# Performance work log

Hardware: AMD Instinct MI355X
Metric: run time of the kernel (lower is better)

Reference implementation:

```python
import jax, jax.numpy as jnp
import numpy as np

B, S, H, E, V = 32, 256, 512, 300, 32000
ALEN, LLEN, POL = 4, 16, 3
HOP, LAM = 10, 0.01


def _layernorm(x, g, b, eps=1e-12):
    mu = jnp.mean(x, -1, keepdims=True)
    var = jnp.mean((x - mu) ** 2, -1, keepdims=True)
    return (x - mu) / jnp.sqrt(var + eps) * g + b


def _pos_weight(x, a0, a1, text_len, aspect_len):
    # vectorized version of ASGCN_NEW.position_weight
    j = jnp.arange(x.shape[1])[None, :]
    cl = (text_len - aspect_len).astype(jnp.float32)[:, None]
    a0b, a1b, tlb = a0[:, None], a1[:, None], text_len[:, None]
    w = jnp.where(j < a0b, 1.0 - (a0b - j) / cl,
        jnp.where(j <= a1b, 0.0,
        jnp.where(j < tlb, 1.0 - (j - a1b) / cl, 0.0)))
    return w[:, :, None] * x


def _mask(x, a0, a1):
    j = jnp.arange(x.shape[1])[None, :]
    m = ((j >= a0[:, None]) & (j <= a1[:, None])).astype(x.dtype)
    return m[:, :, None] * x


def _gcn(x, adj, w, b):
    h = jnp.einsum('bsh,hk->bsk', x, w)
    denom = jnp.sum(adj, 2, keepdims=True) + 1.0
    return jnp.einsum('bst,bth->bsh', adj, h) / denom + b


def _conv1d(x, w, b):
    # x: [B,S,C] -> conv over S with kernel 3, pad 1 -> [B,S,C]
    y = jax.lax.conv_general_dilated(jnp.swapaxes(x, 1, 2), w, (1,), ((1, 1),),
                                     dimension_numbers=('NCH', 'OIH', 'NCH'))
    return jnp.swapaxes(y + b[None, :, None], 1, 2)


def _lstm_dir(x, mask, wih, whh, b, reverse):
    # masked LSTM matching pack_padded semantics: state frozen / output zero at pad
    xs = jnp.swapaxes(x, 0, 1)       # [S,B,E]
    ms = jnp.swapaxes(mask, 0, 1)    # [S,B] bool
    if reverse:
        xs, ms = xs[::-1], ms[::-1]
    pre = jnp.einsum('sbe,ge->sbg', xs, wih) + b
    h0 = jnp.zeros((x.shape[0], whh.shape[1]), x.dtype)

    def step(carry, inp):
        h, c = carry
        p, m = inp
        g = p + h @ whh.T
        i, f, gg, o = jnp.split(g, 4, -1)
        c_new = jax.nn.sigmoid(f) * c + jax.nn.sigmoid(i) * jnp.tanh(gg)
        h_new = jax.nn.sigmoid(o) * jnp.tanh(c_new)
        m_ = m[:, None]
        return (jnp.where(m_, h_new, h), jnp.where(m_, c_new, c)), jnp.where(m_, h_new, 0.0)

    _, ys = jax.lax.scan(step, (h0, h0), (pre, ms))
    if reverse:
        ys = ys[::-1]
    return jnp.swapaxes(ys, 0, 1)


def _hop_attend(m, text_out, g, b):
    tT = jnp.swapaxes(text_out, 1, 2)
    for _ in range(HOP - 1):
        alpha = jnp.einsum('bsh,bht->bst', m, tT)          # [B,S,S]
        a = jnp.einsum('bst,bth->bsh', alpha, text_out)    # [B,S,H]
        m = LAM * _layernorm(jax.nn.sigmoid(a), g, b) + m
    alpha_mat = jnp.einsum('bsh,bht->bst', m, tT)
    alpha = jax.nn.softmax(jnp.sum(alpha_mat, 1, keepdims=True), axis=2)  # [B,1,S]
    return jnp.einsum('bot,bth->boh', alpha, text_out)[:, 0]              # [B,H]


def setup_inputs() -> dict:
    key = jax.random.key(0)
    ks = jax.random.split(key, 20)
    sc = 0.05
    text_indices = jax.random.randint(ks[0], (B, S), 1, V)
    aspect_indices = jax.random.randint(ks[1], (B, ALEN), 1, V)
    left_indices = jax.random.randint(ks[2], (B, LLEN), 1, V)
    adj = (jax.random.uniform(ks[3], (B, S, S)) < 0.1).astype(jnp.float32)
    adj = jnp.minimum(adj + jnp.eye(S, dtype=jnp.float32)[None], 1.0)
    return {
        'text_indices': text_indices,
        'aspect_indices': aspect_indices,
        'left_indices': left_indices,
        'adj': adj,
        'embedding': jax.random.normal(ks[4], (V, E)) * sc,
        'lstm_wih_f': jax.random.normal(ks[5], (4 * H, E)) * sc,
        'lstm_whh_f': jax.random.normal(ks[6], (4 * H, H)) * sc,
        'lstm_b_f': jnp.zeros((4 * H,), jnp.float32),
        'lstm_wih_b': jax.random.normal(ks[7], (4 * H, E)) * sc,
        'lstm_whh_b': jax.random.normal(ks[8], (4 * H, H)) * sc,
        'lstm_b_b': jnp.zeros((4 * H,), jnp.float32),
        'gc_w': jax.random.normal(ks[9], (6, H, H)) * sc,
        'gc_b': jnp.zeros((6, H), jnp.float32),
        'conv1_w': jax.random.normal(ks[10], (H, H, 3)) * sc,
        'conv1_b': jnp.zeros((H,), jnp.float32),
        'conv2_w': jax.random.normal(ks[11], (H, H, 3)) * sc,
        'conv2_b': jnp.zeros((H,), jnp.float32),
        'fc2_w': jax.random.normal(ks[12], (POL, 3 * H)) * sc,
        'fc2_b': jnp.zeros((POL,), jnp.float32),
        'ln_g': jnp.ones((3, H), jnp.float32),
        'ln_b': jnp.zeros((3, H), jnp.float32),
    }


def _forward(text_indices, aspect_indices, left_indices, adj, embedding,
             lstm_wih_f, lstm_whh_f, lstm_b_f, lstm_wih_b, lstm_whh_b, lstm_b_b,
             gc_w, gc_b, conv1_w, conv1_b, conv2_w, conv2_b, fc2_w, fc2_b, ln_g, ln_b):
    text_len = jnp.sum(text_indices != 0, -1)
    aspect_len = jnp.sum(aspect_indices != 0, -1)
    left_len = jnp.sum(left_indices != 0, -1)
    a0 = left_len
    a1 = left_len + aspect_len - 1
    text = embedding[text_indices]  # dropout identity in eval mode
    m = text_indices != 0
    hf = _lstm_dir(text, m, lstm_wih_f, lstm_whh_f, lstm_b_f, False)
    hb = _lstm_dir(text, m, lstm_wih_b, lstm_whh_b, lstm_b_b, True)
    # concat fwd/bwd then reshape(B,S,H,2).mean(-1), exactly as the torch code
    text_out = jnp.concatenate([hf, hb], -1).reshape(B, S, H, 2).mean(-1)

    pw = lambda t: _pos_weight(t, a0, a1, text_len, aspect_len)

    x_conv = jax.nn.relu(_conv1d(pw(text_out), conv1_w, conv1_b))
    x_conv = jax.nn.relu(_conv1d(pw(x_conv), conv2_w, conv2_b))

    x = jax.nn.relu(_gcn(pw(text_out), adj, gc_w[0], gc_b[0]))
    pwx = pw(x)
    graph_mask = jnp.zeros_like(x)
    for k in range(1, 6):
        graph_mask = graph_mask + _mask(jax.nn.relu(_gcn(pwx, adj, gc_w[k], gc_b[k])), a0, a1)

    a1_vec = _hop_attend(graph_mask, text_out, ln_g[0], ln_b[0])
    a2_vec = _hop_attend(_mask(text_out, a0, a1), text_out, ln_g[1], ln_b[1])
    a3_vec = _hop_attend(_mask(x_conv, a0, a1), text_out, ln_g[2], ln_b[2])

    fnout = jnp.concatenate([a1_vec, a2_vec, a3_vec], 1)  # [B, 3H]
    return fnout @ fc2_w.T + fc2_b


def reference(text_indices, aspect_indices, left_indices, adj, embedding,
              lstm_wih_f, lstm_whh_f, lstm_b_f, lstm_wih_b, lstm_whh_b, lstm_b_b,
              gc_w, gc_b, conv1_w, conv1_b, conv2_w, conv2_b, fc2_w, fc2_b, ln_g, ln_b):
    return _forward(text_indices, aspect_indices, left_indices, adj, embedding,
                    lstm_wih_f, lstm_whh_f, lstm_b_f, lstm_wih_b, lstm_whh_b, lstm_b_b,
                    gc_w, gc_b, conv1_w, conv1_b, conv2_w, conv2_b, fc2_w, fc2_b, ln_g, ln_b)
```

## Files before the change

kernel.cpp:

```cpp
#include <hip/hip_runtime.h>
#include <hip/hip_fp16.h>

typedef unsigned int u32;
typedef unsigned long long u64;

static constexpr size_t OFF_X2    = 0;
static constexpr size_t OFF_PRE   = 9830400;
static constexpr size_t OFF_MB    = 131072;
static constexpr size_t OFF_FLG   = 135168;
static constexpr size_t OFF_TOUT  = 0;
static constexpr size_t OFF_TOUTT = 16777216;
static constexpr size_t OFF_PWT   = 33554432;
static constexpr size_t OFF_PWTTH = 50331648;
static constexpr size_t OFF_PWTTL = 58720256;
static constexpr size_t OFF_Y     = 76939264;
static constexpr size_t OFF_AGG0  = 76939264;
static constexpr size_t OFF_GCWT  = 93716480;
static constexpr size_t OFF_PWX   = 110493696;
static constexpr size_t OFF_WD    = 127270912;
static constexpr size_t OFF_WIH   = 131465216;
static constexpr size_t OFF_BIA   = 136380416;
static constexpr size_t OFF_W1T   = 136396800;
static constexpr size_t OFF_W2T   = 139542528;
static constexpr size_t OFF_META  = 142688256;
// ... 163 lines not shown

    const int srow = tid >> 4;
    const int sj   = tid & 15;

    for (int kb = 0; kb < 10; ++kb) {
        #pragma unroll
        for (int i = 0; i < 8; ++i) {
            int row = srow + i*16;
            As2[sj*132 + row] = X2u[(size_t)(m0 + row)*160 + kb*16 + sj];
            Bs2[sj*132 + row] = Wihu[(size_t)(n0 + row)*160 + kb*16 + sj];
        }
        __syncthreads();

        U4H8 bf[4];
        #pragma unroll
        for (int nt = 0; nt < 4; ++nt) {
            int col = wn*64 + nt*16 + l15;
            bf[nt].u = make_uint4(Bs2[(2*q)*132 + col], Bs2[(2*q+1)*132 + col],
                                  Bs2[(2*q+8)*132 + col], Bs2[(2*q+9)*132 + col]);
        }
        #pragma unroll
        for (int mt = 0; mt < 4; ++mt) {
            int row = wm*64 + mt*16 + l15;
            U4H8 af;
            af.u = make_uint4(As2[(2*q)*132 + row], As2[(2*q+1)*132 + row],
                              As2[(2*q+8)*132 + row], As2[(2*q+9)*132 + row]);
            #pragma unroll
            for (int nt = 0; nt < 4; ++nt)
                acc[mt][nt] = __builtin_amdgcn_mfma_f32_16x16x32_f16(af.h, bf[nt].h, acc[mt][nt], 0, 0, 0);
        }
        __syncthreads();
    }

    #pragma unroll
    for (int nt = 0; nt < 4; ++nt) {
        int col = n0 + wn*64 + nt*16 + l15;
        float bv = bias[col];
        #pragma unroll
        for (int mt = 0; mt < 4; ++mt) {
            int rbase = m0 + wm*64 + mt*16 + q*4;
            #pragma unroll
            for (int p = 0; p < 4; ++p)
                pre[(size_t)(rbase + p)*4096 + col] = __float2half(acc[mt][nt][p] + bv);
        }
    }
}

template<int SPLITA, int EPI>
__global__ __launch_bounds__(256)
void mmsplit_k(const float* __restrict__ A, const u32* __restrict__ Bhi,
               const u32* __restrict__ Blo, float* __restrict__ C,
               int N, int Ku32, long sA, long sB, long sC,
               const float* __restrict__ bias, const float* __restrict__ denom,
               const float* __restrict__ posw)
{
    __shared__ u32 Ah[16*132];
    __shared__ u32 Al[16*132];
    __shared__ u32 Bh[16*132];
    __shared__ u32 Bl[16*132];
    const int z = blockIdx.z;
    A   += (size_t)z * sA;
    Bhi += (size_t)z * sB;
    Blo += (size_t)z * sB;
    C   += (size_t)z * sC;
    const int m0 = blockIdx.x * 128;
    const int n0 = blockIdx.y * 128;
    const int tid = threadIdx.x;
    const int wv = tid >> 6;
    const int l  = tid & 63;
    const int q  = l >> 4;
    const int l15 = l & 15;
    const int wm = wv & 1, wn = wv >> 1;
    const int pitchA = 2*Ku32;

    f32x4 acc[4][4];
    #pragma unroll
    for (int mt = 0; mt < 4; ++mt)
        #pragma unroll
        for (int nt = 0; nt < 4; ++nt)
            acc[mt][nt] = (f32x4){0.f, 0.f, 0.f, 0.f};

    const int srow = tid >> 4;
    const int sj   = tid & 15;
    const int nkb = Ku32 >> 4;

    for (int kb = 0; kb < nkb; ++kb) {
        #pragma unroll
        for (int i = 0; i < 8; ++i) {
            int row = srow + i*16;
            float2 av = *(const float2*)(A + (size_t)(m0 + row)*pitchA + kb*32 + 2*sj);
            __half h0 = __float2half(av.x), h1 = __float2half(av.y);
            Ah[sj*132 + row] = (u32)__half_as_ushort(h0) | ((u32)__half_as_ushort(h1) << 16);
            if (SPLITA)
                Al[sj*132 + row] = packh2(av.x - __half2float(h0), av.y - __half2float(h1));
            Bh[sj*132 + row] = Bhi[(size_t)(n0 + row)*Ku32 + kb*16 + sj];
            Bl[sj*132 + row] = Blo[(size_t)(n0 + row)*Ku32 + kb*16 + sj];
        }
        __syncthreads();

        U4H8 bfh[4], bfl[4];
        #pragma unroll
        for (int nt = 0; nt < 4; ++nt) {
            int col = wn*64 + nt*16 + l15;
            bfh[nt].u = make_uint4(Bh[(2*q)*132 + col], Bh[(2*q+1)*132 + col],
                                   Bh[(2*q+8)*132 + col], Bh[(2*q+9)*132 + col]);
            bfl[nt].u = make_uint4(Bl[(2*q)*132 + col], Bl[(2*q+1)*132 + col],
                                   Bl[(2*q+8)*132 + col], Bl[(2*q+9)*132 + col]);
        }
        #pragma unroll
        for (int mt = 0; mt < 4; ++mt) {
            int row = wm*64 + mt*16 + l15;
            U4H8 afh;
            afh.u = make_uint4(Ah[(2*q)*132 + row], Ah[(2*q+1)*132 + row],
                               Ah[(2*q+8)*132 + row], Ah[(2*q+9)*132 + row]);
            #pragma unroll
            for (int nt = 0; nt < 4; ++nt) {
                acc[mt][nt] = __builtin_amdgcn_mfma_f32_16x16x32_f16(afh.h, bfh[nt].h, acc[mt][nt], 0, 0, 0);
                acc[mt][nt] = __builtin_amdgcn_mfma_f32_16x16x32_f16(afh.h, bfl[nt].h, acc[mt][nt], 0, 0, 0);
            }
            if (SPLITA) {
                U4H8 afl;
                afl.u = make_uint4(Al[(2*q)*132 + row], Al[(2*q+1)*132 + row],
                                   Al[(2*q+8)*132 + row], Al[(2*q+9)*132 + row]);
                #pragma unroll
                for (int nt = 0; nt < 4; ++nt)
                    acc[mt][nt] = __builtin_amdgcn_mfma_f32_16x16x32_f16(afl.h, bfh[nt].h, acc[mt][nt], 0, 0, 0);
            }
        }
        __syncthreads();
    }

    #pragma unroll
    for (int nt = 0; nt < 4; ++nt) {
        int col = n0 + wn*64 + nt*16 + l15;
        float bv = (EPI == 1) ? bias[col] : 0.f;
        #pragma unroll
        for (int mt = 0; mt < 4; ++mt) {
            int rbase = m0 + wm*64 + mt*16 + q*4;
            #pragma unroll
            for (int p = 0; p < 4; ++p) {
                int m = rbase + p;
                if (EPI == 0) {
                    C[(size_t)m*N + col] = acc[mt][nt][p];
                } else {
                    float v = fmaf(acc[mt][nt][p], 1.f/denom[m], bv);
                    C[(size_t)m*N + col] = fmaxf(v, 0.f) * posw[m];
                }
            }
        }
    }
}

__global__ __launch_bounds__(256, 1)
void lstm_scan6_k(const __half* __restrict__ pre, const u32* __restrict__ Wmf,
                  const u32* __restrict__ mb, float* __restrict__ y,
                  u32* __restrict__ flags, u64* __restrict__ Hs)
{
    __shared__ u32 hs[32*264];
    __shared__ float gred[4352];

    const int tid = threadIdx.x;
    const int wv = tid >> 6;
    const int l  = tid & 63;
    const int q  = l >> 4;
    const int l15 = l & 15;
    const int dir = blockIdx.x & 1;
    const int g   = blockIdx.x >> 1;
    const int b2 = tid >> 3;
    const int jj = tid & 7;
    const int gcol = g*8 + jj;

    half8 afr[2][4];
    {
        const uint4* wp = (const uint4*)(Wmf + ((((size_t)dir*64 + g)*4 + wv)*2048)) + l;
        #pragma unroll
        for (int mt = 0; mt < 2; ++mt)
            #pragma unroll
            for (int c = 0; c < 4; ++c)
                afr[mt][c] = __builtin_bit_cast(half8, wp[(mt*4 + c)*64]);
    }

    float hreg = 0.f, creg = 0.f;

    const int s0 = dir ? 255 : 0;
    __half ph[4];
    #pragma unroll
    for (int gt = 0; gt < 4; ++gt)
        ph[gt] = pre[((size_t)s0*32 + b2)*4096 + dir*2048 + gt*512 + gcol];
    u32 mbv = mb[s0];

    const int ks64 = wv*64;
    const int srow = tid >> 3, scol = tid & 7;

    for (int t = 0; t < 256; ++t) {
        const int s = dir ? (255 - t) : t;

        if (t == 0) {
            u32* dst = &hs[srow*264 + scol*4];
            #pragma unroll
            for (int i = 0; i < 8; ++i) *(uint4*)(dst + i*32) = make_uint4(0u,0u,0u,0u);
        } else {
            if (tid < 64) {
                u32* fp = flags + (size_t)t*128 + dir*64 + tid;
                int guard = 0;
                u32 fv = __hip_atomic_fetch_add(fp, 0u, __ATOMIC_RELAXED, __HIP_MEMORY_SCOPE_AGENT);
                while (!__all(fv != 0u)) {
                    __builtin_amdgcn_s_sleep(1);
                    fv = __hip_atomic_fetch_add(fp, 0u, __ATOMIC_RELAXED, __HIP_MEMORY_SCOPE_AGENT);
                    if (++guard > (1 << 22)) break;
                }
            }
            __syncthreads();
            int bi = (int)(__brev((u32)t) >> 24);
            const uint4* src = (const uint4*)(Hs + ((size_t)(bi*2 + dir)*32)*128);
            const uint4* tp = src + srow*64 + scol;
            uint4 vv[8];
            #pragma unroll
            for (int i = 0; i < 8; ++i) vv[i] = tp[i*8];
            u32* dst = &hs[srow*264 + scol*4];
            #pragma unroll
            for (int i = 0; i < 8; ++i) *(uint4*)(dst + i*32) = vv[i];
        }
        __syncthreads();

        f32x4 acc[2][2];
        #pragma unroll
        for (int mt = 0; mt < 2; ++mt)
            #pragma unroll
            for (int nt = 0; nt < 2; ++nt)
                acc[mt][nt] = (f32x4){0.f, 0.f, 0.f, 0.f};
        #pragma unroll
        for (int c = 0; c < 4; ++c) {
            #pragma unroll
            for (int nt = 0; nt < 2; ++nt) {
                int base = (nt*16 + l15)*264 + ks64 + c*16 + 2*q;
                uint4 bw = make_uint4(hs[base], hs[base+1], hs[base+8], hs[base+9]);
                half8 bfr = __builtin_bit_cast(half8, bw);
                acc[0][nt] = __builtin_amdgcn_mfma_f32_16x16x32_f16(afr[0][c], bfr, acc[0][nt], 0, 0, 0);
                acc[1][nt] = __builtin_amdgcn_mfma_f32_16x16x32_f16(afr[1][c], bfr, acc[1][nt], 0, 0, 0);
            }
        }

        #pragma unroll
        for (int mt = 0; mt < 2; ++mt)
            #pragma unroll
            for (int nt = 0; nt < 2; ++nt)
                #pragma unroll
                for (int p = 0; p < 4; ++p)
                    gred[(((wv*2 + mt)*2 + nt)*16 + q*4 + p)*17 + l15] = acc[mt][nt][p];
        __syncthreads();

        float gv[4];
        #pragma unroll
        for (int gt = 0; gt < 4; ++gt) {
            int ml = 4*jj + gt;
            int mt = ml >> 4, r = ml & 15;
            int ntile = b2 >> 4, n = b2 & 15;
            float sum = 0.f;
            #pragma unroll
            for (int w2 = 0; w2 < 4; ++w2)
                sum += gred[(((w2*2 + mt)*2 + ntile)*16 + r)*17 + n];
            gv[gt] = sum + __half2float(ph[gt]);
        }
        float cn = sigf(gv[1])*creg + sigf(gv[0])*tanhf(gv[2]);
        float hn = sigf(gv[3])*tanhf(cn);
        bool mk = (mbv >> b2) & 1u;
        if (mk) { hreg = hn; creg = cn; }

        {
            int l4 = l & ~3;
            float h0 = __shfl(hreg, l4 + 0);
            float h1 = __shfl(hreg, l4 + 1);
            float h2 = __shfl(hreg, l4 + 2);
            float h3 = __shfl(hreg, l4 + 3);
            if ((tid & 3) == 0) {
                u64 pk = (u64)packh2(h0, h1) | ((u64)packh2(h2, h3) << 32);
                int bi2 = (int)(__brev((u32)(t + 1)) >> 24);
                int wsel = (tid >> 2) & 1;
                __hip_atomic_store(&Hs[((size_t)(bi2*2 + dir)*32 + b2)*128 + 2*g + wsel], pk,
                                   __ATOMIC_RELAXED, __HIP_MEMORY_SCOPE_AGENT);
            }
        }
        asm volatile("s_waitcnt vmcnt(0)" ::: "memory");
        __syncthreads();
        if (tid == 0) {
            __hip_atomic_store(flags + (size_t)(t + 1)*128 + dir*64 + g, 1u,
                               __ATOMIC_RELAXED, __HIP_MEMORY_SCOPE_AGENT);
        }
        y[(((size_t)dir*32 + b2)*256 + s)*512 + gcol] = mk ? hn : 0.f;

        if (t < 255) {
            int sn = dir ? (254 - t) : (t + 1);
            #pragma unroll
            for (int gt = 0; gt < 4; ++gt)
                ph[gt] = pre[((size_t)sn*32 + b2)*4096 + dir*2048 + gt*512 + gcol];
            mbv = mb[sn];
        }
    }
}

__global__ __launch_bounds__(256)
void fuse_ct_k(const float* __restrict__ y, const float* __restrict__ posw,
               float* __restrict__ text_out, float* __restrict__ pw_text,
               float* __restrict__ tOutT, u32* __restrict__ pwtThi, u32* __restrict__ pwtTlo)
{
    __shared__ float tileV[32][33];
    __shared__ float tileP[32][33];
    int b = blockIdx.z, s0 = blockIdx.x*32, h0 = blockIdx.y*32;
    int tx = threadIdx.x & 31, ty4 = threadIdx.x >> 5;
    int hg = h0 + tx;
    #pragma unroll
    for (int rr = 0; rr < 4; ++rr) {
        int sy = ty4 + rr*8;
        int s = s0 + sy;
        const float* p;
        if (hg < 256) p = y + (((size_t)b*256 + s)*512 + 2*hg);
        else          p = y + (((size_t)(32 + b)*256 + s)*512 + 2*(hg - 256));
        float v = 0.5f*(p[0] + p[1]);
        float pw = v * posw[b*256 + s];
        text_out[((size_t)b*256 + s)*512 + hg] = v;
        pw_text [((size_t)b*256 + s)*512 + hg] = pw;
        tileV[sy][tx] = v;
        tileP[sy][tx] = pw;
    }
    __syncthreads();
    #pragma unroll
    for (int rr = 0; rr < 4; ++rr) {
        int hy = ty4 + rr*8;
        tOutT[((size_t)b*512 + h0 + hy)*256 + s0 + tx] = tileV[tx][hy];
    }
    for (int slot = threadIdx.x; slot < 512; slot += 256) {
        int hh = slot >> 4, sp = slot & 15;
        float p0 = tileP[2*sp][hh];
        float p1 = tileP[2*sp + 1][hh];
        __half q0 = __float2half(p0), q1 = __float2half(p1);
        size_t di = ((size_t)b*512 + h0 + hh)*128 + (s0 >> 1) + sp;
        pwtThi[di] = (u32)__half_as_ushort(q0) | ((u32)__half_as_ushort(q1) << 16);
        pwtTlo[di] = packh2(p0 - __half2float(q0), p1 - __half2float(q1));
    }
}

__global__ __launch_bounds__(256)
void aggm_k(const float* __restrict__ adj, const float* __restrict__ pwx,
            const int* __restrict__ meta, float* __restrict__ aggm)
{
    int b = blockIdx.x >> 2, r = blockIdx.x & 3;
    int a0 = meta[b], nm = meta[64+b];
    int s = a0 + r; if (s > 255) s = 255;
    __shared__ float arow[256];
    int tid = threadIdx.x;
    arow[tid] = adj[((size_t)b*256 + s)*256 + tid];
    __syncthreads();
    float acc0 = 0.f, acc1 = 0.f;
    for (int t = 0; t < 256; ++t) {
        float av = arow[t];
        acc0 = fmaf(av, pwx[((size_t)b*256 + t)*512 + tid], acc0);
        acc1 = fmaf(av, pwx[((size_t)b*256 + t)*512 + tid + 256], acc1);
    }
    bool ok = (r < nm);
    aggm[((size_t)b*4 + r)*512 + tid]       = ok ? acc0 : 0.f;
    aggm[((size_t)b*4 + r)*512 + tid + 256] = ok ? acc1 : 0.f;
}

__global__ __launch_bounds__(256)
void gmaskn_k(const float* __restrict__ aggm, const float* __restrict__ gcw,
              const float* __restrict__ gcb, const int* __restrict__ meta,
              const float* __restrict__ denom, float* __restrict__ gmsk)
{
    int b = blockIdx.x >> 1, hf = blockIdx.x & 1;
    int col = hf*256 + threadIdx.x;
    int a0 = meta[b], nm = meta[64+b];
    __shared__ float rows[4][512];
    int tid = threadIdx.x;
    #pragma unroll
    for (int r = 0; r < 4; ++r) {
        rows[r][tid]       = aggm[((size_t)b*4 + r)*512 + tid];
        rows[r][tid + 256] = aggm[((size_t)b*4 + r)*512 + tid + 256];
    }
    float inv[4];
    #pragma unroll
    for (int r = 0; r < 4; ++r) {
        int srow = a0 + r; if (srow > 255) srow = 255;
        inv[r] = 1.f / denom[b*256 + srow];
    }
    __syncthreads();
    float gm[4] = {0.f, 0.f, 0.f, 0.f};
    for (int k = 1; k <= 5; ++k) {
        const float* w = gcw + (size_t)k*262144 + col;
        float bb = gcb[k*512 + col];
        float ak[4] = {0.f, 0.f, 0.f, 0.f};
        for (int c = 0; c < 512; ++c) {
            float wv = w[(size_t)c*512];
            #pragma unroll
            for (int r = 0; r < 4; ++r) ak[r] = fmaf(rows[r][c], wv, ak[r]);
        }
        #pragma unroll
        for (int r = 0; r < 4; ++r) gm[r] += fmaxf(fmaf(ak[r], inv[r], bb), 0.f);
    }
    #pragma unroll
    for (int r = 0; r < 4; ++r)
        gmsk[((size_t)b*4 + r)*512 + col] = (r < nm) ? gm[r] : 0.f;
}

__global__ __launch_bounds__(256)
void conv1n_k(const float* __restrict__ pwt, const float* __restrict__ w1T,
              const float* __restrict__ b1, const int* __restrict__ meta,
              const float* __restrict__ posw, float* __restrict__ c1pw)
{
    int b = blockIdx.x >> 1, hf = blockIdx.x & 1;
    int col = hf*256 + threadIdx.x;
    int a0 = meta[b];
    __shared__ float rows[8][512];
    int tid = threadIdx.x;
    #pragma unroll
    for (int i = 0; i < 8; ++i) {
        int si = a0 - 2 + i;
        bool v = (si >= 0 && si < 256);
        rows[i][tid]       = v ? pwt[((size_t)b*256 + si)*512 + tid]       : 0.f;
        rows[i][tid + 256] = v ? pwt[((size_t)b*256 + si)*512 + tid + 256] : 0.f;
    }
    __syncthreads();
    float bv = b1[col];
    float acc[6] = {bv, bv, bv, bv, bv, bv};
    #pragma unroll
    for (int kk = 0; kk < 3; ++kk) {
        const float* w = w1T + (size_t)kk*262144 + col;
        for (int c = 0; c < 512; ++c) {
            float wv = w[(size_t)c*512];
            #pragma unroll
            for (int r = 0; r < 6; ++r) acc[r] = fmaf(rows[r + kk][c], wv, acc[r]);
        }
    }
    #pragma unroll
    for (int r = 0; r < 6; ++r) {
        int s = a0 - 1 + r;
        bool valid = (s >= 0 && s < 256);
        float pv = valid ? posw[b*256 + s] : 0.f;
        c1pw[((size_t)b*6 + r)*512 + col] = valid ? fmaxf(acc[r], 0.f)*pv : 0.f;
    }
}

__global__ __launch_bounds__(256)
void conv2n_k(const float* __restrict__ c1pw, const float* __restrict__ w2T,
              const float* __restrict__ b2, const int* __restrict__ meta,
              float* __restrict__ xc2)
{
    int b = blockIdx.x >> 1, hf = blockIdx.x & 1;
    int col = hf*256 + threadIdx.x;
    int nm = meta[64+b];
    __shared__ float rows[6][512];
    int tid = threadIdx.x;
    #pragma unroll
    for (int i = 0; i < 6; ++i) {
        rows[i][tid]       = c1pw[((size_t)b*6 + i)*512 + tid];
        rows[i][tid + 256] = c1pw[((size_t)b*6 + i)*512 + tid + 256];
    }
    __syncthreads();
    float bv = b2[col];
    float acc[4] = {bv, bv, bv, bv};
    #pragma unroll
    for (int kk = 0; kk < 3; ++kk) {
        const float* w = w2T + (size_t)kk*262144 + col;
        for (int c = 0; c < 512; ++c) {
            float wv = w[(size_t)c*512];
            #pragma unroll
            for (int r = 0; r < 4; ++r) acc[r] = fmaf(rows[r + kk][c], wv, acc[r]);
        }
    }
    #pragma unroll
    for (int r = 0; r < 4; ++r)
        xc2[((size_t)b*4 + r)*512 + col] = (r < nm) ? fmaxf(acc[r], 0.f) : 0.f;
}

__global__ __launch_bounds__(1024)
void attend_k(const float* __restrict__ text_out, const float* __restrict__ tOutT,
              const float* __restrict__ gmsk, const float* __restrict__ xc2,
              const int* __restrict__ meta,
              const float* __restrict__ lng, const float* __restrict__ lnb,
              float* __restrict__ avec)
{
    __shared__ float m5[5][512];
    __shared__ float alpha[5][256];
    __shared__ float part[5120];
    __shared__ float wt[256];
    __shared__ float msum[512];
    __shared__ float red[16];
    int b = blockIdx.x, att = blockIdx.y;
    int tid = threadIdx.x;
    int a0 = meta[b], nm = meta[64+b];
    float lgam = 0.f, lbet = 0.f;
    if (tid < 512) {
        #pragma unroll
        for (int r = 0; r < 4; ++r) {
            float v = 0.f;
            if (r < nm) {
                if (att == 0)      v = gmsk[((size_t)b*4 + r)*512 + tid];
                else if (att == 1) v = text_out[((size_t)b*256 + a0 + r)*512 + tid];
                else               v = xc2[((size_t)b*4 + r)*512 + tid];
            }
            m5[r][tid] = v;
        }
        m5[4][tid] = 0.f;
        lgam = lng[att*512 + tid]; lbet = lnb[att*512 + tid];
    }
    const float* tT = tOutT + (size_t)b*512*256;
    const float* tO = text_out + (size_t)b*256*512;
    __syncthreads();

    for (int hop = 0; hop < 9; ++hop) {
        {
            int t = tid & 255, hq = tid >> 8;
            float a5[5] = {0.f, 0.f, 0.f, 0.f, 0.f};
            const float* tp = tT + (size_t)(hq*128)*256 + t;
            for (int h = 0; h < 128; ++h) {
                float v = tp[(size_t)h*256];
                int hh = hq*128 + h;
                #pragma unroll
                for (int r = 0; r < 5; ++r) a5[r] = fmaf(m5[r][hh], v, a5[r]);
            }
            #pragma unroll
            for (int r = 0; r < 5; ++r) part[(hq*5 + r)*256 + t] = a5[r];
        }
        __syncthreads();
        for (int idx = tid; idx < 1280; idx += 1024) {
            int r = idx >> 8, t2 = idx & 255;
            alpha[r][t2] = part[(0*5+r)*256+t2] + part[(1*5+r)*256+t2]
                         + part[(2*5+r)*256+t2] + part[(3*5+r)*256+t2];
        }
        __syncthreads();
        {
            int hh = tid & 511, hf2 = tid >> 9;
            float a5[5] = {0.f, 0.f, 0.f, 0.f, 0.f};
            const float* tp0 = tO + (size_t)(hf2*128)*512 + hh;
            for (int t = 0; t < 128; ++t) {
                float v = tp0[(size_t)t*512];
                #pragma unroll
                for (int r = 0; r < 5; ++r) a5[r] = fmaf(alpha[r][hf2*128 + t], v, a5[r]);
            }
            #pragma unroll
            for (int r = 0; r < 5; ++r) part[(hf2*5 + r)*512 + hh] = a5[r];
        }
        __syncthreads();
        #pragma unroll 1
        for (int r = 0; r < 5; ++r) {
            bool act = tid < 512;
            float xv = 0.f;
            if (act) xv = sigf(part[(0*5+r)*512 + tid] + part[(1*5+r)*512 + tid]);
            float s1 = act ? xv : 0.f;
            #pragma unroll
            for (int off = 1; off < 64; off <<= 1) s1 += __shfl_xor(s1, off);
            if ((tid & 63) == 0) red[tid >> 6] = s1;
            __syncthreads();
            float mu = (red[0]+red[1]+red[2]+red[3]+red[4]+red[5]+red[6]+red[7]) * (1.f/512.f);
            __syncthreads();
            float d = xv - mu;
            float s2 = act ? d*d : 0.f;
            #pragma unroll
            for (int off = 1; off < 64; off <<= 1) s2 += __shfl_xor(s2, off);
            if ((tid & 63) == 0) red[tid >> 6] = s2;
            __syncthreads();
            float var = (red[0]+red[1]+red[2]+red[3]+red[4]+red[5]+red[6]+red[7]) * (1.f/512.f);
            __syncthreads();
            if (act) {
                float ln = d * rsqrtf(var + 1e-12f) * lgam + lbet;
                if (r < nm || r == 4) m5[r][tid] += 0.01f * ln;
            }
        }
        __syncthreads();
    }
    if (tid < 512) {
        float ms = 0.f;
        #pragma unroll
        for (int r = 0; r < 4; ++r) if (r < nm) ms += m5[r][tid];
        ms += (float)(256 - nm) * m5[4][tid];
        msum[tid] = ms;
    }
    __syncthreads();
    {
        int t = tid & 255, hq = tid >> 8;
        float sc = 0.f;
        const float* tp = tT + (size_t)(hq*128)*256 + t;
        for (int h = 0; h < 128; ++h) sc = fmaf(msum[hq*128 + h], tp[(size_t)h*256], sc);
        part[hq*256 + t] = sc;
    }
    __syncthreads();
    float sv = -3.0e38f;
    if (tid < 256) sv = part[tid] + part[256+tid] + part[512+tid] + part[768+tid];
    float mx = sv;
    #pragma unroll
    for (int off = 1; off < 64; off <<= 1) mx = fmaxf(mx, __shfl_xor(mx, off));
    if ((tid & 63) == 0) red[tid >> 6] = mx;
    __syncthreads();
    mx = fmaxf(fmaxf(red[0], red[1]), fmaxf(red[2], red[3]));
    __syncthreads();
    float ex = (tid < 256) ? expf(sv - mx) : 0.f;
    float ss = ex;
    #pragma unroll
    for (int off = 1; off < 64; off <<= 1) ss += __shfl_xor(ss, off);
    if ((tid & 63) == 0) red[tid >> 6] = ss;
    __syncthreads();
    float tot = red[0]+red[1]+red[2]+red[3];
    __syncthreads();
    if (tid < 256) wt[tid] = ex / tot;
    __syncthreads();
    {
        int hh = tid & 511, hf2 = tid >> 9;
        float acc = 0.f;
        const float* tp0 = tO + (size_t)(hf2*128)*512 + hh;
        for (int t = 0; t < 128; ++t) acc = fmaf(wt[hf2*128 + t], tp0[(size_t)t*512], acc);
        part[hf2*512 + hh] = acc;
    }
    __syncthreads();
    if (tid < 512)
        avec[((size_t)att*32 + b)*512 + tid] = part[tid] + part[512 + tid];
}

__global__ __launch_bounds__(128)
void final_k(const float* __restrict__ avec, const float* __restrict__ fw,
             const float* __restrict__ fbb, float* __restrict__ out)
{
    int b = blockIdx.x, tid = threadIdx.x;
    float a0 = 0.f, a1 = 0.f, a2 = 0.f;
    for (int j = tid; j < 1536; j += 128) {
        float v = avec[((size_t)(j >> 9)*32 + b)*512 + (j & 511)];
        a0 = fmaf(v, fw[j], a0);
        a1 = fmaf(v, fw[1536 + j], a1);
        a2 = fmaf(v, fw[3072 + j], a2);
    }
    #pragma unroll
    for (int off = 1; off < 64; off <<= 1) {
        a0 += __shfl_xor(a0, off); a1 += __shfl_xor(a1, off); a2 += __shfl_xor(a2, off);
    }
    __shared__ float red[6];
    if ((tid & 63) == 0) { int w = tid >> 6; red[w] = a0; red[2+w] = a1; red[4+w] = a2; }
    __syncthreads();
    if (tid == 0) {
        out[b*3+0] = red[0] + red[1] + fbb[0];
        out[b*3+1] = red[2] + red[3] + fbb[1];
        out[b*3+2] = red[4] + red[5] + fbb[2];
    }
}

extern "C" void kernel_launch(void* const* d_in, const int* in_sizes, int n_in,
                              void* d_out, int out_size, void* d_ws, size_t ws_size,
                              hipStream_t stream)
{
    (void)in_sizes; (void)n_in; (void)out_size;
    if (ws_size < WS_NEED) return;
    const int*   ti    = (const int*)d_in[0];
    const int*   ai    = (const int*)d_in[1];
    const int*   li    = (const int*)d_in[2];
    const float* adj   = (const float*)d_in[3];
    const float* emb   = (const float*)d_in[4];
    const float* wih_f = (const float*)d_in[5];
    const float* whh_f = (const float*)d_in[6];
    const float* b_f   = (const float*)d_in[7];
    const float* wih_b = (const float*)d_in[8];
    const float* whh_b = (const float*)d_in[9];
    const float* b_b   = (const float*)d_in[10];
    const float* gcw   = (const float*)d_in[11];
    const float* gcb   = (const float*)d_in[12];
    const float* c1w   = (const float*)d_in[13];
    const float* c1b   = (const float*)d_in[14];
    const float* c2w   = (const float*)d_in[15];
    const float* c2b   = (const float*)d_in[16];
    const float* fw    = (const float*)d_in[17];
    const float* fb    = (const float*)d_in[18];
    const float* lng   = (const float*)d_in[19];
    const float* lnb   = (const float*)d_in[20];

    char* ws = (char*)d_ws;
    __half* X2h      = (__half*)(ws + OFF_X2);
    __half* pre      = (__half*)(ws + OFF_PRE);
    u32*    mb       = (u32*)(ws + OFF_MB);
    u32*    flags    = (u32*)(ws + OFF_FLG);
    float*  text_out = (float*)(ws + OFF_TOUT);
    float*  tOutT    = (float*)(ws + OFF_TOUTT);
    float*  pw_text  = (float*)(ws + OFF_PWT);
    u32*    pwtThi   = (u32*)(ws + OFF_PWTTH);
    u32*    pwtTlo   = (u32*)(ws + OFF_PWTTL);
    float*  y        = (float*)(ws + OFF_Y);
    float*  agg0     = (float*)(ws + OFF_AGG0);
    u32*    Ghi      = (u32*)(ws + OFF_GCWT);
    u32*    Glo      = (u32*)(ws + OFF_GCWT + 524288);
    float*  pwx      = (float*)(ws + OFF_PWX);
    u64*    Hs       = (u64*)(ws + OFF_PWX);
    u32*    Wmf      = (u32*)(ws + OFF_WD);
    u32*    Wih      = (u32*)(ws + OFF_WIH);
    float*  biascat  = (float*)(ws + OFF_BIA);
    float*  w1T      = (float*)(ws + OFF_W1T);
    float*  w2T      = (float*)(ws + OFF_W2T);
    int*    meta     = (int*)(ws + OFF_META);
    float*  clf      = (float*)(ws + OFF_CLF);
    float*  denom    = (float*)(ws + OFF_DEN);
    float*  posw     = (float*)(ws + OFF_POSW);
    float*  aggm     = (float*)(ws + OFF_AGGM);
    float*  gmsk     = (float*)(ws + OFF_GMSK);
    float*  c1pw     = (float*)(ws + OFF_C1PW);
    float*  xc2      = (float*)(ws + OFF_XC2);
    float*  avec     = (float*)(ws + OFF_AVEC);

    len_k<<<1, 64, 0, stream>>>(ti, ai, li, meta, clf);
    pd_k<<<8192, 256, 0, stream>>>(adj, meta, clf, denom, posw);
    gather_k<<<8192, 128, 0, stream>>>(ti, emb, X2h);
    wpackih_k<<<2560, 256, 0, stream>>>(wih_f, wih_b, Wih);
    wmf_k<<<4096, 256, 0, stream>>>(whh_f, whh_b, Wmf);
    wtrans_k<<<dim3(3072, 2), 256, 0, stream>>>(c1w, c2w, w1T, w2T);
    hipMemcpyAsync(biascat,        b_f, 2048*4, hipMemcpyDeviceToDevice, stream);
    hipMemcpyAsync(biascat + 2048, b_b, 2048*4, hipMemcpyDeviceToDevice, stream);

    pre_mfma_k<<<dim3(64, 32), 256, 0, stream>>>((const u32*)X2h, Wih, biascat, pre);

    maskb_k<<<1, 256, 0, stream>>>(ti, mb);
    hipMemsetAsync(flags, 0, (size_t)257*128*4, stream);

    lstm_scan6_k<<<128, 256, 0, stream>>>(pre, Wmf, mb, y, flags, Hs);

    fuse_ct_k<<<dim3(8, 16, 32), 256, 0, stream>>>(y, posw, text_out, pw_text,
                                                   tOutT, pwtThi, pwtTlo);
    mmsplit_k<0, 0><<<dim3(2, 4, 32), 256, 0, stream>>>(adj, pwtThi, pwtTlo, agg0,
        512, 128, 65536L, 65536L, 131072L, nullptr, nullptr, nullptr);
    wpackg_k<<<512, 256, 0, stream>>>(gcw, Ghi, Glo);
    mmsplit_k<1, 1><<<dim3(64, 4, 1), 256, 0, stream>>>(agg0, Ghi, Glo, pwx,
        512, 256, 0L, 0L, 0L, gcb, denom, posw);

    aggm_k<<<128, 256, 0, stream>>>(adj, pwx, meta, aggm);
    gmaskn_k<<<64, 256, 0, stream>>>(aggm, gcw, gcb, meta, denom, gmsk);
    conv1n_k<<<64, 256, 0, stream>>>(pw_text, w1T, c1b, meta, posw, c1pw);
    conv2n_k<<<64, 256, 0, stream>>>(c1pw, w2T, c2b, meta, xc2);
    attend_k<<<dim3(32, 3), 1024, 0, stream>>>(text_out, tOutT, gmsk, xc2, meta, lng, lnb, avec);
    final_k<<<32, 128, 0, stream>>>(avec, fw, fb, (float*)d_out);
}
```

Baseline: 1.496 ms.

## Merge forward and backward LSTM directions into one workgroup per gate slice

The recurrent LSTM scan now launches 64 workgroups instead of 128, and each one handles both directions in turn, keeping weight fragments for both in registers. Each wave now waits only on its own 16 producer flags and copies its own K-slice of the hidden state into LDS. This drops the extra block-wide barrier that used to follow the flag wait. The aim is to cut cross-block synchronisation cost and let the wait for one direction overlap work on the other. The cost is that the two directions run one after the other inside a block, so each timestep has a longer dependent chain and register pressure is higher.

```diff
diff --git a/kernel.cpp b/kernel.cpp
--- a/kernel.cpp
+++ b/kernel.cpp
@@ -339,7 +339,7 @@
 }
 
 __global__ __launch_bounds__(256, 1)
-void lstm_scan6_k(const __half* __restrict__ pre, const u32* __restrict__ Wmf,
+void lstm_scan7_k(const __half* __restrict__ pre, const u32* __restrict__ Wmf,
                   const u32* __restrict__ mb, float* __restrict__ y,
                   u32* __restrict__ flags, u64* __restrict__ Hs)
 {
@@ -351,137 +351,145 @@
     const int l  = tid & 63;
     const int q  = l >> 4;
     const int l15 = l & 15;
-    const int dir = blockIdx.x & 1;
-    const int g   = blockIdx.x >> 1;
+    const int g  = blockIdx.x;
     const int b2 = tid >> 3;
     const int jj = tid & 7;
     const int gcol = g*8 + jj;
-
-    half8 afr[2][4];
-    {
-        const uint4* wp = (const uint4*)(Wmf + ((((size_t)dir*64 + g)*4 + wv)*2048)) + l;
+    const int ks64 = wv*64;
+    const int sb = l >> 1;
+    const int sh = l & 1;
+
+    half8 afr[2][2][4];
+    #pragma unroll
+    for (int d = 0; d < 2; ++d) {
+        const uint4* wp = (const uint4*)(Wmf + ((((size_t)d*64 + g)*4 + wv)*2048)) + l;
         #pragma unroll
         for (int mt = 0; mt < 2; ++mt)
             #pragma unroll
             for (int c = 0; c < 4; ++c)
-                afr[mt][c] = __builtin_bit_cast(half8, wp[(mt*4 + c)*64]);
-    }
-
-    float hreg = 0.f, creg = 0.f;
-
-    const int s0 = dir ? 255 : 0;
-    __half ph[4];
-    #pragma unroll
-    for (int gt = 0; gt < 4; ++gt)
-        ph[gt] = pre[((size_t)s0*32 + b2)*4096 + dir*2048 + gt*512 + gcol];
-    u32 mbv = mb[s0];
-
-    const int ks64 = wv*64;
-    const int srow = tid >> 3, scol = tid & 7;
+                afr[d][mt][c] = __builtin_bit_cast(half8, wp[(mt*4 + c)*64]);
+    }
+
+    float hreg[2] = {0.f, 0.f}, creg[2] = {0.f, 0.f};
+    __half ph[2][4];
+    #pragma unroll
+    for (int d = 0; d < 2; ++d) {
+        int s0 = d ? 255 : 0;
+        #pragma unroll
+        for (int gt = 0; gt < 4; ++gt)
+            ph[d][gt] = pre[((size_t)s0*32 + b2)*4096 + d*2048 + gt*512 + gcol];
+    }
+    u32 mbv[2] = {mb[0], mb[255]};
 
     for (int t = 0; t < 256; ++t) {
-        const int s = dir ? (255 - t) : t;
-
-        if (t == 0) {
-            u32* dst = &hs[srow*264 + scol*4];
-            #pragma unroll
-            for (int i = 0; i < 8; ++i) *(uint4*)(dst + i*32) = make_uint4(0u,0u,0u,0u);
-        } else {
-            if (tid < 64) {
-                u32* fp = flags + (size_t)t*128 + dir*64 + tid;
+        const int bi  = (int)(__brev((u32)t) >> 24);
+        const int bi2 = (int)(__brev((u32)(t + 1)) >> 24);
+
+        #pragma unroll 1
+        for (int d = 0; d < 2; ++d) {
+            const int s = d ? (255 - t) : t;
+
+            if (t == 0) {
+                u32* dst = &hs[sb*264 + ks64 + sh*32];
+                #pragma unroll
+                for (int i = 0; i < 8; ++i) *(uint4*)(dst + i*4) = make_uint4(0u,0u,0u,0u);
+            } else {
+                u32 fv = 1u;
+                u32* fp = flags + (size_t)t*128 + d*64 + wv*16 + (l & 15);
+                if (l < 16)
+                    fv = __hip_atomic_fetch_add(fp, 0u, __ATOMIC_RELAXED, __HIP_MEMORY_SCOPE_AGENT);
                 int guard = 0;
-                u32 fv = __hip_atomic_fetch_add(fp, 0u, __ATOMIC_RELAXED, __HIP_MEMORY_SCOPE_AGENT);
                 while (!__all(fv != 0u)) {
                     __builtin_amdgcn_s_sleep(1);
-                    fv = __hip_atomic_fetch_add(fp, 0u, __ATOMIC_RELAXED, __HIP_MEMORY_SCOPE_AGENT);
+                    if (l < 16)
+                        fv = __hip_atomic_fetch_add(fp, 0u, __ATOMIC_RELAXED, __HIP_MEMORY_SCOPE_AGENT);
                     if (++guard > (1 << 22)) break;
                 }
-            }
+                const uint4* srcrow = (const uint4*)(Hs + ((size_t)(bi*2 + d)*32 + sb)*128)
+                                      + wv*16 + sh*8;
+                uint4 vv[8];
+                #pragma unroll
+                for (int i = 0; i < 8; ++i) vv[i] = srcrow[i];
+                u32* dst = &hs[sb*264 + ks64 + sh*32];
+                #pragma unroll
+                for (int i = 0; i < 8; ++i) *(uint4*)(dst + i*4) = vv[i];
+            }
+
+            f32x4 acc[2][2];
+            #pragma unroll
+            for (int mt = 0; mt < 2; ++mt)
+                #pragma unroll
+                for (int nt = 0; nt < 2; ++nt)
+                    acc[mt][nt] = (f32x4){0.f, 0.f, 0.f, 0.f};
+            #pragma unroll
+            for (int c = 0; c < 4; ++c) {
+                #pragma unroll
+                for (int nt = 0; nt < 2; ++nt) {
+                    int base = (nt*16 + l15)*264 + ks64 + c*16 + 2*q;
+                    uint4 bw = make_uint4(hs[base], hs[base+1], hs[base+8], hs[base+9]);
+                    half8 bfr = __builtin_bit_cast(half8, bw);
+                    acc[0][nt] = __builtin_amdgcn_mfma_f32_16x16x32_f16(afr[d][0][c], bfr, acc[0][nt], 0, 0, 0);
+                    acc[1][nt] = __builtin_amdgcn_mfma_f32_16x16x32_f16(afr[d][1][c], bfr, acc[1][nt], 0, 0, 0);
+                }
+            }
+            #pragma unroll
+            for (int mt = 0; mt < 2; ++mt)
+                #pragma unroll
+                for (int nt = 0; nt < 2; ++nt)
+                    #pragma unroll
+                    for (int p = 0; p < 4; ++p)
+                        gred[(((wv*2 + mt)*2 + nt)*16 + q*4 + p)*17 + l15] = acc[mt][nt][p];
             __syncthreads();
-            int bi = (int)(__brev((u32)t) >> 24);
-            const uint4* src = (const uint4*)(Hs + ((size_t)(bi*2 + dir)*32)*128);
-            const uint4* tp = src + srow*64 + scol;
-            uint4 vv[8];
-            #pragma unroll
-            for (int i = 0; i < 8; ++i) vv[i] = tp[i*8];
-            u32* dst = &hs[srow*264 + scol*4];
-            #pragma unroll
-            for (int i = 0; i < 8; ++i) *(uint4*)(dst + i*32) = vv[i];
-        }
-        __syncthreads();
-
-        f32x4 acc[2][2];
-        #pragma unroll
-        for (int mt = 0; mt < 2; ++mt)
-            #pragma unroll
-            for (int nt = 0; nt < 2; ++nt)
-                acc[mt][nt] = (f32x4){0.f, 0.f, 0.f, 0.f};
-        #pragma unroll
-        for (int c = 0; c < 4; ++c) {
-            #pragma unroll
-            for (int nt = 0; nt < 2; ++nt) {
-                int base = (nt*16 + l15)*264 + ks64 + c*16 + 2*q;
-                uint4 bw = make_uint4(hs[base], hs[base+1], hs[base+8], hs[base+9]);
-                half8 bfr = __builtin_bit_cast(half8, bw);
-                acc[0][nt] = __builtin_amdgcn_mfma_f32_16x16x32_f16(afr[0][c], bfr, acc[0][nt], 0, 0, 0);
-                acc[1][nt] = __builtin_amdgcn_mfma_f32_16x16x32_f16(afr[1][c], bfr, acc[1][nt], 0, 0, 0);
-            }
-        }
-
-        #pragma unroll
-        for (int mt = 0; mt < 2; ++mt)
-            #pragma unroll
-            for (int nt = 0; nt < 2; ++nt)
-                #pragma unroll
-                for (int p = 0; p < 4; ++p)
-                    gred[(((wv*2 + mt)*2 + nt)*16 + q*4 + p)*17 + l15] = acc[mt][nt][p];
-        __syncthreads();
-
-        float gv[4];
-        #pragma unroll
-        for (int gt = 0; gt < 4; ++gt) {
-            int ml = 4*jj + gt;
-            int mt = ml >> 4, r = ml & 15;
-            int ntile = b2 >> 4, n = b2 & 15;
-            float sum = 0.f;
-            #pragma unroll
-            for (int w2 = 0; w2 < 4; ++w2)
-                sum += gred[(((w2*2 + mt)*2 + ntile)*16 + r)*17 + n];
-            gv[gt] = sum + __half2float(ph[gt]);
-        }
-        float cn = sigf(gv[1])*creg + sigf(gv[0])*tanhf(gv[2]);
-        float hn = sigf(gv[3])*tanhf(cn);
-        bool mk = (mbv >> b2) & 1u;
-        if (mk) { hreg = hn; creg = cn; }
-
-        {
-            int l4 = l & ~3;
-            float h0 = __shfl(hreg, l4 + 0);
-            float h1 = __shfl(hreg, l4 + 1);
-            float h2 = __shfl(hreg, l4 + 2);
-            float h3 = __shfl(hreg, l4 + 3);
-            if ((tid & 3) == 0) {
-                u64 pk = (u64)packh2(h0, h1) | ((u64)packh2(h2, h3) << 32);
-                int bi2 = (int)(__brev((u32)(t + 1)) >> 24);
-                int wsel = (tid >> 2) & 1;
-                __hip_atomic_store(&Hs[((size_t)(bi2*2 + dir)*32 + b2)*128 + 2*g + wsel], pk,
+
+            float gv[4];
+            #pragma unroll
+            for (int gt = 0; gt < 4; ++gt) {
+                int ml = 4*jj + gt;
+                int mt = ml >> 4, r = ml & 15;
+                int ntile = b2 >> 4, n = b2 & 15;
+                float sum = 0.f;
+                #pragma unroll
+                for (int w2 = 0; w2 < 4; ++w2)
+                    sum += gred[(((w2*2 + mt)*2 + ntile)*16 + r)*17 + n];
+                gv[gt] = sum + __half2float(ph[d][gt]);
+            }
+            float cn = sigf(gv[1])*creg[d] + sigf(gv[0])*tanhf(gv[2]);
+            float hn = sigf(gv[3])*tanhf(cn);
+            bool mk = (mbv[d] >> b2) & 1u;
+            if (mk) { hreg[d] = hn; creg[d] = cn; }
+
+            {
+                int l4 = l & ~3;
+                float h0 = __shfl(hreg[d], l4 + 0);
+                float h1 = __shfl(hreg[d], l4 + 1);
+                float h2 = __shfl(hreg[d], l4 + 2);
+                float h3 = __shfl(hreg[d], l4 + 3);
+                if ((tid & 3) == 0) {
+                    u64 pk = (u64)packh2(h0, h1) | ((u64)packh2(h2, h3) << 32);
+                    int wsel = (tid >> 2) & 1;
+                    __hip_atomic_store(&Hs[((size_t)(bi2*2 + d)*32 + b2)*128 + 2*g + wsel], pk,
+                                       __ATOMIC_RELAXED, __HIP_MEMORY_SCOPE_AGENT);
+                }
+            }
+            asm volatile("s_waitcnt vmcnt(0)" ::: "memory");
+            __syncthreads();
+            if (tid == 0) {
+                __hip_atomic_store(flags + (size_t)(t + 1)*128 + d*64 + g, 1u,
                                    __ATOMIC_RELAXED, __HIP_MEMORY_SCOPE_AGENT);
             }
-        }
-        asm volatile("s_waitcnt vmcnt(0)" ::: "memory");
-        __syncthreads();
-        if (tid == 0) {
-            __hip_atomic_store(flags + (size_t)(t + 1)*128 + dir*64 + g, 1u,
-                               __ATOMIC_RELAXED, __HIP_MEMORY_SCOPE_AGENT);
-        }
-        y[(((size_t)dir*32 + b2)*256 + s)*512 + gcol] = mk ? hn : 0.f;
+            y[(((size_t)d*32 + b2)*256 + s)*512 + gcol] = mk ? hn : 0.f;
+        }
 
         if (t < 255) {
-            int sn = dir ? (254 - t) : (t + 1);
-            #pragma unroll
-            for (int gt = 0; gt < 4; ++gt)
-                ph[gt] = pre[((size_t)sn*32 + b2)*4096 + dir*2048 + gt*512 + gcol];
-            mbv = mb[sn];
+            #pragma unroll
+            for (int d = 0; d < 2; ++d) {
+                int sn = d ? (254 - t) : (t + 1);
+                #pragma unroll
+                for (int gt = 0; gt < 4; ++gt)
+                    ph[d][gt] = pre[((size_t)sn*32 + b2)*4096 + d*2048 + gt*512 + gcol];
+            }
+            mbv[0] = mb[t + 1];
+            mbv[1] = mb[254 - t];
         }
     }
 }
@@ -901,7 +909,7 @@
     maskb_k<<<1, 256, 0, stream>>>(ti, mb);
     hipMemsetAsync(flags, 0, (size_t)257*128*4, stream);
 
-    lstm_scan6_k<<<128, 256, 0, stream>>>(pre, Wmf, mb, y, flags, Hs);
+    lstm_scan7_k<<<64, 256, 0, stream>>>(pre, Wmf, mb, y, flags, Hs);
 
     fuse_ct_k<<<dim3(8, 16, 32), 256, 0, stream>>>(y, posw, text_out, pw_text,
                                                    tOutT, pwtThi, pwtTlo);
```

Result: slower. 2.467 ms (+64.9%).

## Per-wave flag polling in LSTM scan and batched layernorm reductions in attend

Applied to the files above, without the earlier changes.

The recurrent LSTM kernel now has each wave poll only the producer flags for its own K-slice of the hidden state. It loads that slice straight into its private region of shared memory. This removes two block-wide barriers per time step from the serial critical path, and the hidden-state exchange buffer is relaid out by gate group so each wave's slice is contiguous. Separately, attend_k computes the five layernorm mean/variance reductions together, cutting the per-hop barrier count from twenty to two at the cost of more registers and shared arrays.

```diff
diff --git a/kernel.cpp b/kernel.cpp
--- a/kernel.cpp
+++ b/kernel.cpp
@@ -339,7 +339,7 @@
 }
 
 __global__ __launch_bounds__(256, 1)
-void lstm_scan6_k(const __half* __restrict__ pre, const u32* __restrict__ Wmf,
+void lstm_scan8_k(const __half* __restrict__ pre, const u32* __restrict__ Wmf,
                   const u32* __restrict__ mb, float* __restrict__ y,
                   u32* __restrict__ flags, u64* __restrict__ Hs)
 {
@@ -356,6 +356,7 @@
     const int b2 = tid >> 3;
     const int jj = tid & 7;
     const int gcol = g*8 + jj;
+    const int ks64 = wv*64;
 
     half8 afr[2][4];
     {
@@ -376,39 +377,40 @@
         ph[gt] = pre[((size_t)s0*32 + b2)*4096 + dir*2048 + gt*512 + gcol];
     u32 mbv = mb[s0];
 
-    const int ks64 = wv*64;
-    const int srow = tid >> 3, scol = tid & 7;
-
     for (int t = 0; t < 256; ++t) {
         const int s = dir ? (255 - t) : t;
 
         if (t == 0) {
-            u32* dst = &hs[srow*264 + scol*4];
-            #pragma unroll
-            for (int i = 0; i < 8; ++i) *(uint4*)(dst + i*32) = make_uint4(0u,0u,0u,0u);
+            #pragma unroll
+            for (int i = 0; i < 8; ++i) {
+                int flat = i*64 + l;
+                int gp = flat >> 5, bb = flat & 31;
+                *(uint4*)&hs[bb*264 + ks64 + 4*gp] = make_uint4(0u,0u,0u,0u);
+            }
         } else {
-            if (tid < 64) {
-                u32* fp = flags + (size_t)t*128 + dir*64 + tid;
-                int guard = 0;
-                u32 fv = __hip_atomic_fetch_add(fp, 0u, __ATOMIC_RELAXED, __HIP_MEMORY_SCOPE_AGENT);
-                while (!__all(fv != 0u)) {
-                    __builtin_amdgcn_s_sleep(1);
+            u32 fv = 1u;
+            u32* fp = flags + (size_t)t*128 + dir*64 + 16*wv + (l & 15);
+            if (l < 16)
+                fv = __hip_atomic_fetch_add(fp, 0u, __ATOMIC_RELAXED, __HIP_MEMORY_SCOPE_AGENT);
+            int guard = 0;
+            while (!__all(fv != 0u)) {
+                __builtin_amdgcn_s_sleep(1);
+                if (l < 16)
                     fv = __hip_atomic_fetch_add(fp, 0u, __ATOMIC_RELAXED, __HIP_MEMORY_SCOPE_AGENT);
-                    if (++guard > (1 << 22)) break;
-                }
-            }
-            __syncthreads();
+                if (++guard > (1 << 22)) break;
+            }
             int bi = (int)(__brev((u32)t) >> 24);
-            const uint4* src = (const uint4*)(Hs + ((size_t)(bi*2 + dir)*32)*128);
-            const uint4* tp = src + srow*64 + scol;
+            const uint4* base = (const uint4*)(Hs + ((size_t)(bi*2 + dir))*4096 + (size_t)(16*wv)*64);
             uint4 vv[8];
             #pragma unroll
-            for (int i = 0; i < 8; ++i) vv[i] = tp[i*8];
-            u32* dst = &hs[srow*264 + scol*4];
-            #pragma unroll
-            for (int i = 0; i < 8; ++i) *(uint4*)(dst + i*32) = vv[i];
-        }
-        __syncthreads();
+            for (int i = 0; i < 8; ++i) vv[i] = base[i*64 + l];
+            #pragma unroll
+            for (int i = 0; i < 8; ++i) {
+                int flat = i*64 + l;
+                int gp = flat >> 5, bb = flat & 31;
+                *(uint4*)&hs[bb*264 + ks64 + 4*gp] = vv[i];
+            }
+        }
 
         f32x4 acc[2][2];
         #pragma unroll
@@ -420,8 +422,8 @@
         for (int c = 0; c < 4; ++c) {
             #pragma unroll
             for (int nt = 0; nt < 2; ++nt) {
-                int base = (nt*16 + l15)*264 + ks64 + c*16 + 2*q;
-                uint4 bw = make_uint4(hs[base], hs[base+1], hs[base+8], hs[base+9]);
+                int base2 = (nt*16 + l15)*264 + ks64 + c*16 + 2*q;
+                uint4 bw = make_uint4(hs[base2], hs[base2+1], hs[base2+8], hs[base2+9]);
                 half8 bfr = __builtin_bit_cast(half8, bw);
                 acc[0][nt] = __builtin_amdgcn_mfma_f32_16x16x32_f16(afr[0][c], bfr, acc[0][nt], 0, 0, 0);
                 acc[1][nt] = __builtin_amdgcn_mfma_f32_16x16x32_f16(afr[1][c], bfr, acc[1][nt], 0, 0, 0);
@@ -464,7 +466,7 @@
                 u64 pk = (u64)packh2(h0, h1) | ((u64)packh2(h2, h3) << 32);
                 int bi2 = (int)(__brev((u32)(t + 1)) >> 24);
                 int wsel = (tid >> 2) & 1;
-                __hip_atomic_store(&Hs[((size_t)(bi2*2 + dir)*32 + b2)*128 + 2*g + wsel], pk,
+                __hip_atomic_store(Hs + ((size_t)(bi2*2 + dir))*4096 + (size_t)g*64 + b2*2 + wsel, pk,
                                    __ATOMIC_RELAXED, __HIP_MEMORY_SCOPE_AGENT);
             }
         }
@@ -672,6 +674,8 @@
     __shared__ float wt[256];
     __shared__ float msum[512];
     __shared__ float red[16];
+    __shared__ float red5a[5][16];
+    __shared__ float red5b[5][16];
     int b = blockIdx.x, att = blockIdx.y;
     int tid = threadIdx.x;
     int a0 = meta[b], nm = meta[64+b];
@@ -728,29 +732,52 @@
             for (int r = 0; r < 5; ++r) part[(hf2*5 + r)*512 + hh] = a5[r];
         }
         __syncthreads();
-        #pragma unroll 1
-        for (int r = 0; r < 5; ++r) {
+        {
             bool act = tid < 512;
-            float xv = 0.f;
-            if (act) xv = sigf(part[(0*5+r)*512 + tid] + part[(1*5+r)*512 + tid]);
-            float s1 = act ? xv : 0.f;
-            #pragma unroll
-            for (int off = 1; off < 64; off <<= 1) s1 += __shfl_xor(s1, off);
-            if ((tid & 63) == 0) red[tid >> 6] = s1;
+            float xv[5], s1[5];
+            #pragma unroll
+            for (int r = 0; r < 5; ++r) {
+                xv[r] = act ? sigf(part[(0*5+r)*512 + tid] + part[(1*5+r)*512 + tid]) : 0.f;
+                s1[r] = xv[r];
+            }
+            #pragma unroll
+            for (int off = 1; off < 64; off <<= 1)
+                #pragma unroll
+                for (int r = 0; r < 5; ++r) s1[r] += __shfl_xor(s1[r], off);
+            if ((tid & 63) == 0) {
+                #pragma unroll
+                for (int r = 0; r < 5; ++r) red5a[r][tid >> 6] = s1[r];
+            }
             __syncthreads();
-            float mu = (red[0]+red[1]+red[2]+red[3]+red[4]+red[5]+red[6]+red[7]) * (1.f/512.f);
-            __syncthreads();
-            float d = xv - mu;
-            float s2 = act ? d*d : 0.f;
-            #pragma unroll
-            for (int off = 1; off < 64; off <<= 1) s2 += __shfl_xor(s2, off);
-            if ((tid & 63) == 0) red[tid >> 6] = s2;
-            __syncthreads();
-            float var = (red[0]+red[1]+red[2]+red[3]+red[4]+red[5]+red[6]+red[7]) * (1.f/512.f);
+            float mu[5], dd[5], s2[5];
+            #pragma unroll
+            for (int r = 0; r < 5; ++r) {
+                float m = 0.f;
+                #pragma unroll
+                for (int w = 0; w < 16; ++w) m += red5a[r][w];
+                mu[r] = m * (1.f/512.f);
+                dd[r] = xv[r] - mu[r];
+                s2[r] = act ? dd[r]*dd[r] : 0.f;
+            }
+            #pragma unroll
+            for (int off = 1; off < 64; off <<= 1)
+                #pragma unroll
+                for (int r = 0; r < 5; ++r) s2[r] += __shfl_xor(s2[r], off);
+            if ((tid & 63) == 0) {
+                #pragma unroll
+                for (int r = 0; r < 5; ++r) red5b[r][tid >> 6] = s2[r];
+            }
             __syncthreads();
             if (act) {
-                float ln = d * rsqrtf(var + 1e-12f) * lgam + lbet;
-                if (r < nm || r == 4) m5[r][tid] += 0.01f * ln;
+                #pragma unroll
+                for (int r = 0; r < 5; ++r) {
+                    float v = 0.f;
+                    #pragma unroll
+                    for (int w = 0; w < 16; ++w) v += red5b[r][w];
+                    float var = v * (1.f/512.f);
+                    float ln = dd[r] * rsqrtf(var + 1e-12f) * lgam + lbet;
+                    if (r < nm || r == 4) m5[r][tid] += 0.01f * ln;
+                }
             }
         }
         __syncthreads();
@@ -901,7 +928,7 @@
     maskb_k<<<1, 256, 0, stream>>>(ti, mb);
     hipMemsetAsync(flags, 0, (size_t)257*128*4, stream);
 
-    lstm_scan6_k<<<128, 256, 0, stream>>>(pre, Wmf, mb, y, flags, Hs);
+    lstm_scan8_k<<<128, 256, 0, stream>>>(pre, Wmf, mb, y, flags, Hs);
 
     fuse_ct_k<<<dim3(8, 16, 32), 256, 0, stream>>>(y, posw, text_out, pw_text,
                                                    tOutT, pwtThi, pwtTlo);
```

Measured after the change: 1.651 ms. +10.3%, slower.
